# Performance work log

Measured on AMD Instinct MI355X. Metric: run time of the kernel, lower is better.

The kernel has to match this reference:

```python
import jax, jax.numpy as jnp
import numpy as np
from jax import lax

N = 1024          # n_ligand == n_receptor == feature dim (required by broadcast in source)
D = 1024          # gnn_input_dim == gnn_output_dim
H = 32            # hopi_output_dim
C = 32            # cnn_channels


def setup_inputs() -> dict:
    key = jax.random.key(0)
    ks = jax.random.split(key, 24)
    s = 0.02
    inp = {
        "ligand_node_features": jax.random.normal(ks[0], (N, D), jnp.float32),
        "ligand_edge_features": jax.random.normal(ks[1], (N, D), jnp.float32),
        "ligand_adjacency": jax.random.uniform(ks[2], (N, N), jnp.float32),
        "receptor_node_features": jax.random.normal(ks[3], (N, D), jnp.float32),
        "receptor_edge_features": jax.random.normal(ks[4], (N, D), jnp.float32),
        "receptor_adjacency": jax.random.uniform(ks[5], (N, N), jnp.float32),
        # GNNLayer params (shared between ligand and receptor, as in source)
        "Wn": jax.random.normal(ks[6], (D, D), jnp.float32) * s,
        "bn": jax.random.normal(ks[7], (D,), jnp.float32) * s,
        "We": jax.random.normal(ks[8], (D, D), jnp.float32) * s,
        "be": jax.random.normal(ks[9], (D,), jnp.float32) * s,
        "Wa": jax.random.normal(ks[10], (1, D), jnp.float32) * s,
        "ba": jax.random.normal(ks[11], (1,), jnp.float32) * s,
        # HighOrderPairwiseInteraction: Linear(2*D -> H)
        "W_hopi": jax.random.normal(ks[12], (H, 2 * D), jnp.float32) * s,
        "b_hopi": jax.random.normal(ks[13], (H,), jnp.float32) * s,
        # CNN tail
        "conv1_w": jax.random.normal(ks[14], (C, H, 3, 3), jnp.float32) * s,
        "conv1_b": jax.random.normal(ks[15], (C,), jnp.float32) * s,
        "conv2_w": jax.random.normal(ks[16], (C, C, 3, 3), jnp.float32) * s,
        "conv2_b": jax.random.normal(ks[17], (C,), jnp.float32) * s,
        "conv3_w": jax.random.normal(ks[18], (1, C, 1, 1), jnp.float32) * s,
        "conv3_b": jax.random.normal(ks[19], (1,), jnp.float32) * s,
    }
    return inp


def _gnn(nf, ef, Wn, bn, We, be, Wa, ba):
    # aggregated: [N, D]
    agg = jnp.tanh(nf @ Wn.T + bn + ef @ We.T + be)
    scores = agg @ Wa.T + ba                      # [N, 1]
    attn = jax.nn.softmax(scores, axis=1)         # softmax over size-1 dim -> ones (faithful)
    weighted = jnp.sum(agg * attn, axis=1)        # [N]
    return nf + weighted                          # [N,D] + [N] broadcasts over last dim (D == N)


def _conv(x, w, b):
    y = lax.conv_general_dilated(x, w, (1, 1), "SAME",
                                 dimension_numbers=("NCHW", "OIHW", "NCHW"))
    return y + b[None, :, None, None]


def reference(ligand_node_features, ligand_edge_features, ligand_adjacency,
              receptor_node_features, receptor_edge_features, receptor_adjacency,
              Wn, bn, We, be, Wa, ba, W_hopi, b_hopi,
              conv1_w, conv1_b, conv2_w, conv2_b, conv3_w, conv3_b):
    lig = _gnn(ligand_node_features, ligand_edge_features, Wn, bn, We, be, Wa, ba)
    rec = _gnn(receptor_node_features, receptor_edge_features, Wn, bn, We, be, Wa, ba)

    # HOPI: interactions[i, j] = Linear(cat(lig[i], rec[j])) == lig[i] @ Wl.T + rec[j] @ Wr.T + b
    Wl, Wr = W_hopi[:, :D], W_hopi[:, D:]
    lig_p = lig @ Wl.T                            # [N, H]
    rec_p = rec @ Wr.T                            # [N, H]
    interactions = lig_p[:, None, :] + rec_p[None, :, :] + b_hopi  # [N, N, H]

    x = jnp.transpose(interactions, (2, 0, 1))[None]  # [1, H, N, N]
    x = jax.nn.relu(_conv(x, conv1_w, conv1_b))
    x = jax.nn.relu(_conv(x, conv2_w, conv2_b))
    x = _conv(x, conv3_w, conv3_b)                # [1, 1, N, N]
    return x[0, 0]                                # [N, N]
```

## Files before the change

kernel.cpp:

```cpp
#include <hip/hip_runtime.h>


typedef _Float16 half8 __attribute__((ext_vector_type(8)));
typedef _Float16 half4 __attribute__((ext_vector_type(4)));
typedef float    f32x4 __attribute__((ext_vector_type(4)));

__device__ __forceinline__ short f2h_bits(float f){
    _Float16 h = (_Float16)f;
    return __builtin_bit_cast(short, h);
}
__device__ __forceinline__ half8 pack2(const float4& x, const float4& y){
    half8 r;
    r[0] = (_Float16)x.x; r[1] = (_Float16)x.y;
    r[2] = (_Float16)x.z; r[3] = (_Float16)x.w;
    r[4] = (_Float16)y.x; r[5] = (_Float16)y.y;
    r[6] = (_Float16)y.z; r[7] = (_Float16)y.w;
    return r;
}
__device__ __forceinline__ half4 pack4(const float4& x){
    half4 r;
    r[0] = (_Float16)x.x; r[1] = (_Float16)x.y;
    r[2] = (_Float16)x.z; r[3] = (_Float16)x.w;
    return r;
}
__device__ __forceinline__ float tanh_fast(float x){
    float e = __expf(2.f * x);
    return 1.f - 2.f / (e + 1.f);
}

#define SWZ(c) ((((c) >> 1) & 3) << 3)

#define GNN_LOAD(AV, BV, KBN) {                                              \
    const int kbn_ = (KBN) & 2047;                                           \
    const float* Asrc_ = (kbn_ < 1024) ? A0 : A1;                            \
    const float* Bsrc_ = (kbn_ < 1024) ? Wn : We;                            \
    const int kk_ = kbn_ & 1023;                                             \
    const float* ap_ = Asrc_ + (size_t)(j0 + arow) * 1024 + kk_ + akc;       \
    const float* bp_ = Bsrc_ + (size_t)(d0 + brow) * 1024 + kk_ + bkc;       \
    AV[0] = *reinterpret_cast<const float4*>(ap_);                           \
    AV[1] = *reinterpret_cast<const float4*>(ap_ + 4);                       \
    AV[2] = *reinterpret_cast<const float4*>(ap_ + 8);                       \
    AV[3] = *reinterpret_cast<const float4*>(ap_ + 12);                      \
    BV[0] = *reinterpret_cast<const float4*>(bp_);                           \
    BV[1] = *reinterpret_cast<const float4*>(bp_ + 4);                       \
}

#define GNN_STAGE(AV, BV) {                                                  \
    const int ga_ = (t & 3) * 2;                                             \
    const int sa_ = arow & 7;                                                \
    *reinterpret_cast<half8*>(&As[arow * 64 + ((ga_    ) ^ sa_) * 8]) = pack2(AV[0], AV[1]); \
    *reinterpret_cast<half8*>(&As[arow * 64 + ((ga_ + 1) ^ sa_) * 8]) = pack2(AV[2], AV[3]); \
    *reinterpret_cast<half8*>(&Bs[brow * 64 + ((t & 7) ^ (brow & 7)) * 8]) = pack2(BV[0], BV[1]); \
}

#define GNN_STAGE_W(KBS) {                                                   \
    const int r32_ = t >> 4;                                                 \
    const int kc_  = (t & 15) * 4;                                           \
    float4 wv_ = *reinterpret_cast<const float4*>(                           \
        Wp + (size_t)r32_ * 2048 + (KBS) + kc_);                             \
    *reinterpret_cast<half4*>(                                               \
        &Bs2[r32_ * 64 + ((((t & 15) >> 1)) ^ (r32_ & 7)) * 8 + (t & 1) * 4]) = pack4(wv_); \
}

#define GNN_MFMA() {                                                         \
    _Pragma("unroll")                                                        \
    for (int ks = 0; ks < 2; ++ks){                                          \
        half8 Af[2], Bf[2];                                                  \
        _Pragma("unroll")                                                    \
        for (int m = 0; m < 2; ++m){                                         \
            int row = wm * 32 + m * 16 + lr;                                 \
            int g   = ((ks * 4 + lg) ^ (row & 7)) * 8;                       \
            Af[m] = *reinterpret_cast<const half8*>(&As[row * 64 + g]);      \
        }                                                                    \
        _Pragma("unroll")                                                    \
        for (int n = 0; n < 2; ++n){                                         \
            int col = wn * 32 + n * 16 + lr;                                 \
            int g   = ((ks * 4 + lg) ^ (col & 7)) * 8;                       \
            Bf[n] = *reinterpret_cast<const half8*>(&Bs[col * 64 + g]);      \
        }                                                                    \
        _Pragma("unroll")                                                    \
        for (int m = 0; m < 2; ++m)                                          \
            _Pragma("unroll")                                                \
            for (int n = 0; n < 2; ++n)                                      \
                acc[m][n] = __builtin_amdgcn_mfma_f32_16x16x32_f16(          \
                    Af[m], Bf[n], acc[m][n], 0, 0, 0);                       \
    }                                                                        \
}

#define GNN_PMFMA() {                                                        \
    _Pragma("unroll")                                                        \
    for (int ks = 0; ks < 2; ++ks){                                          \
        int prow = wid * 16 + lr;                                            \
        half8 Af = *reinterpret_cast<const half8*>(                          \
            &As[prow * 64 + ((ks * 4 + lg) ^ (prow & 7)) * 8]);              \
        _Pragma("unroll")                                                    \
        for (int n = 0; n < 2; ++n){                                         \
            int col = n * 16 + lr;                                           \
            half8 Bf2 = *reinterpret_cast<const half8*>(                     \
                &Bs2[col * 64 + ((ks * 4 + lg) ^ (col & 7)) * 8]);           \
            pacc[n] = __builtin_amdgcn_mfma_f32_16x16x32_f16(                \
                Af, Bf2, pacc[n], 0, 0, 0);                                  \
        }                                                                    \
    }                                                                        \
}

__global__ __launch_bounds__(512) void gnn_kernel(
    const float* __restrict__ lig_nf, const float* __restrict__ lig_ef,
    const float* __restrict__ rec_nf, const float* __restrict__ rec_ef,
    const float* __restrict__ Wn, const float* __restrict__ We,
    const float* __restrict__ bn, const float* __restrict__ be,
    const float* __restrict__ W_hopi,
    float* __restrict__ part,
    short* __restrict__ Pw)
{
    __shared__ __attribute__((aligned(16))) short As[128 * 64];
    __shared__ __attribute__((aligned(16))) short Bs[64 * 64];
    __shared__ __attribute__((aligned(16))) short Bs2[32 * 64];
    __shared__ float red[128][2];

    const int t  = threadIdx.x;
    const int cx = blockIdx.z;
    const float* A0 = cx ? rec_nf : lig_nf;
    const float* A1 = cx ? rec_ef : lig_ef;
    const float* Wp = W_hopi + (cx ? 1024 : 0);
    const int j0 = blockIdx.x * 128;
    const int d0 = blockIdx.y * 64;
    const bool doP = (blockIdx.y == 0);

    const int wid  = t >> 6;
    const int wm   = wid >> 1;
    const int wn   = wid & 1;
    const int lane = t & 63;
    const int lr   = lane & 15;
    const int lg   = lane >> 4;

    f32x4 acc[2][2];
    #pragma unroll
    for (int m = 0; m < 2; ++m)
        #pragma unroll
        for (int n = 0; n < 2; ++n)
            acc[m][n] = (f32x4){0.f, 0.f, 0.f, 0.f};
    f32x4 pacc[2];
    pacc[0] = (f32x4){0.f, 0.f, 0.f, 0.f};
    pacc[1] = (f32x4){0.f, 0.f, 0.f, 0.f};

    const int arow = t >> 2;
    const int akc  = (t & 3) * 16;
    const int brow = t >> 3;
    const int bkc  = (t & 7) * 8;

    float4 avA[4], bvA[2], avB[4], bvB[2];
    GNN_LOAD(avA, bvA, 0);
    GNN_LOAD(avB, bvB, 64);

    for (int kb = 0; kb < 2048; kb += 128){
        const bool pA = doP && (kb < 1024);
        const bool pB = doP && (kb + 64 < 1024);
        __syncthreads();
        GNN_STAGE(avA, bvA);
        if (pA) GNN_STAGE_W(kb);
        GNN_LOAD(avA, bvA, kb + 128);
        __syncthreads();
        GNN_MFMA();
        if (pA) GNN_PMFMA();
        __syncthreads();
        GNN_STAGE(avB, bvB);
        if (pB) GNN_STAGE_W(kb + 64);
        GNN_LOAD(avB, bvB, kb + 192);
        __syncthreads();
        GNN_MFMA();
        if (pB) GNN_PMFMA();
    }

    float rowsum[2][4];
    #pragma unroll
    for (int m = 0; m < 2; ++m)
        #pragma unroll
        for (int jj = 0; jj < 4; ++jj) rowsum[m][jj] = 0.f;
    #pragma unroll
    for (int n = 0; n < 2; ++n){
        int d = d0 + wn * 32 + n * 16 + lr;
        float bias = bn[d] + be[d];
        #pragma unroll
        for (int m = 0; m < 2; ++m)
            #pragma unroll
            for (int jj = 0; jj < 4; ++jj)
                rowsum[m][jj] += tanh_fast(acc[m][n][jj] + bias);
    }
    #pragma unroll
    for (int mask = 1; mask < 16; mask <<= 1)
        #pragma unroll
        for (int m = 0; m < 2; ++m)
            #pragma unroll
            for (int jj = 0; jj < 4; ++jj)
                rowsum[m][jj] += __shfl_xor(rowsum[m][jj], mask);
    __syncthreads();
    if (lr == 0){
        #pragma unroll
        for (int m = 0; m < 2; ++m)
            #pragma unroll
            for (int jj = 0; jj < 4; ++jj)
                red[wm * 32 + m * 16 + lg * 4 + jj][wn] = rowsum[m][jj];
    }
    __syncthreads();
    if (t < 128)
        part[(size_t)cx * 16384 + (size_t)blockIdx.y * 1024 + j0 + t]
            = red[t][0] + red[t][1];

    if (doP){
        #pragma unroll
        for (int n = 0; n < 2; ++n)
            #pragma unroll
            for (int jj = 0; jj < 4; ++jj){
                int grow = j0 + wid * 16 + lg * 4 + jj;
                Pw[(size_t)cx * 32768 + (size_t)grow * 32 + n * 16 + lr]
                    = f2h_bits(pacc[n][jj]);
            }
    }
}

__global__ __launch_bounds__(512) void pp2_kernel(
    const float* __restrict__ W_hopi, const float* __restrict__ b_hopi,
    const float* __restrict__ w1, const float* __restrict__ b1,
    const float* __restrict__ w2,
    const float* __restrict__ part, const short* __restrict__ Pw,
    float* __restrict__ Kp, short* __restrict__ U16, short* __restrict__ V16,
    short* __restrict__ w2f16)
{
    __shared__ __attribute__((aligned(16))) char smem[47232];
    const int t = threadIdx.x;
    const int role = blockIdx.x;

    if (role < 32){
        short* Pz = reinterpret_cast<short*>(smem);
        short* Ws = reinterpret_cast<short*>(smem + 5376);

        const int cx = role >> 4;
        const int r0 = (role & 15) * 64;
        short* O = cx ? V16 : U16;
        const short* Psrc = Pw + (size_t)cx * 32768;

        const int wid = t >> 6;
        const int lane = t & 63;
        const int lr = lane & 15;
        const int lg = lane >> 4;

        for (int idx = t; idx < 2112; idx += 512){
            int l = idx >> 5;
            int h = idx & 31;
            int gr = r0 - 1 + l;
            short v = 0;
            if ((unsigned)gr < 1024u) v = Psrc[(size_t)gr * 32 + h];
            Pz[l * 40 + h] = v;
        }

        #pragma unroll
        for (int q = 0; q < 2; ++q){
            int pr = t * 2 + q;
            int co = pr >> 5;
            int ci = pr & 31;
            const float* wp = w1 + co * 288 + ci * 9;
            float tap[9];
            #pragma unroll
            for (int e = 0; e < 9; ++e) tap[e] = wp[e];
            #pragma unroll
            for (int d = 0; d < 3; ++d){
                float ta, tb, tc;
                if (cx == 0){ ta = tap[d * 3 + 0]; tb = tap[d * 3 + 1]; tc = tap[d * 3 + 2]; }
                else        { ta = tap[0 + d];     tb = tap[3 + d];     tc = tap[6 + d]; }
                Ws[(0 * 32 + co) * 104 + d * 32 + ci] = f2h_bits(ta + tb + tc);
                Ws[(1 * 32 + co) * 104 + d * 32 + ci] = f2h_bits(tb + tc);
                Ws[(2 * 32 + co) * 104 + d * 32 + ci] = f2h_bits(ta + tb);
            }
        }
        __syncthreads();

        if (wid < 4){
            f32x4 uacc[3][2];
            #pragma unroll
            for (int cs = 0; cs < 3; ++cs)
                #pragma unroll
                for (int n = 0; n < 2; ++n)
                    uacc[cs][n] = (f32x4){0.f, 0.f, 0.f, 0.f};
            #pragma unroll
            for (int d = 0; d < 3; ++d){
                int ar = wid * 16 + lr;
                half8 Ap = *reinterpret_cast<const half8*>(
                    &Pz[(ar + d) * 40 + lg * 8]);
                #pragma unroll
                for (int cs = 0; cs < 3; ++cs)
                    #pragma unroll
                    for (int n = 0; n < 2; ++n){
                        half8 Bp = *reinterpret_cast<const half8*>(
                            &Ws[(cs * 32 + n * 16 + lr) * 104 + d * 32 + lg * 8]);
                        uacc[cs][n] = __builtin_amdgcn_mfma_f32_16x16x32_f16(
                            Ap, Bp, uacc[cs][n], 0, 0, 0);
                    }
            }
            #pragma unroll
            for (int cs = 0; cs < 3; ++cs)
                #pragma unroll
                for (int n = 0; n < 2; ++n)
                    #pragma unroll
                    for (int jj = 0; jj < 4; ++jj){
                        int grow = r0 + wid * 16 + lg * 4 + jj;
                        O[((size_t)(cs << 10) + grow) * 32 + n * 16 + lr]
                            = f2h_bits(uacc[cs][n][jj]);
                    }
        }
        return;
    }

    if (role == 33){
        #pragma unroll
        for (int q = 0; q < 18; ++q){
            int e = t + q * 512;
            int co  = e / 288;
            int rem = e - co * 288;
            int ci  = rem / 9;
            int tap = rem - ci * 9;
            w2f16[(tap * 32 + co) * 32 + (ci ^ SWZ(co))] = f2h_bits(w2[e]);
        }
        return;
    }

    float* ws_l = reinterpret_cast<float*>(smem);
    float* ws_r = reinterpret_cast<float*>(smem + 4096);
    float* red  = reinterpret_cast<float*>(smem + 8192);
    float* cvs  = reinterpret_cast<float*>(smem + 10240);
    float* w1s  = reinterpret_cast<float*>(smem + 10368);

    #pragma unroll
    for (int q = 0; q < 5; ++q){
        int i4 = t + q * 512;
        if (i4 < 2304)
            *reinterpret_cast<float4*>(&w1s[i4 * 4]) =
                *reinterpret_cast<const float4*>(w1 + i4 * 4);
    }
    for (int j = t; j < 1024; j += 512){
        float sl = 0.f, sr = 0.f;
        #pragma unroll
        for (int b = 0; b < 16; ++b){
            sl += part[b * 1024 + j];
            sr += part[16384 + b * 1024 + j];
        }
        ws_l[j] = sl; ws_r[j] = sr;
    }
    __syncthreads();
    {
        const int h = t & 31;
        const int seg = t >> 5;
        const float* wl = W_hopi + (size_t)h * 2048 + seg * 64;
        const float* wr = wl + 1024;
        float s = 0.f;
        #pragma unroll 8
        for (int j = 0; j < 64; j += 4){
            float4 a = *reinterpret_cast<const float4*>(wl + j);
            float4 b = *reinterpret_cast<const float4*>(wr + j);
            const float* l = &ws_l[seg * 64 + j];
            const float* r = &ws_r[seg * 64 + j];
            s = fmaf(l[0], a.x, s); s = fmaf(l[1], a.y, s);
            s = fmaf(l[2], a.z, s); s = fmaf(l[3], a.w, s);
            s = fmaf(r[0], b.x, s); s = fmaf(r[1], b.y, s);
            s = fmaf(r[2], b.z, s); s = fmaf(r[3], b.w, s);
        }
        red[t] = s;
    }
    __syncthreads();
    if (t < 32){
        float tot = b_hopi[t];
        #pragma unroll
        for (int g = 0; g < 16; ++g) tot += red[g * 32 + t];
        cvs[t] = tot;
    }
    __syncthreads();
    for (int e = t; e < 288; e += 512){
        int co  = e & 31;
        int cse = e >> 5;
        int yc  = cse / 3, xc = cse - yc * 3;
        float sum = b1[co];
        for (int ci = 0; ci < 32; ++ci){
            const float* wp = &w1s[co * 288 + ci * 9];
            float t00 = wp[0], t01 = wp[1], t02 = wp[2];
            float t10 = wp[3], t11 = wp[4], t12 = wp[5];
            float t20 = wp[6], t21 = wp[7], t22 = wp[8];
            float r0, r1, r2;
            if (xc == 0){ r0 = t00+t01+t02; r1 = t10+t11+t12; r2 = t20+t21+t22; }
            else if (xc == 1){ r0 = t01+t02; r1 = t11+t12; r2 = t21+t22; }
            else { r0 = t00+t01; r1 = t10+t11; r2 = t20+t21; }
            float wsum = (yc == 0) ? (r0+r1+r2) : ((yc == 1) ? (r1+r2) : (r0+r1));
            sum = fmaf(cvs[ci], wsum, sum);
        }
        Kp[cse * 32 + co] = sum;
    }
}

__global__ __launch_bounds__(512) void conv_kernel(
    const short* __restrict__ U16, const short* __restrict__ V16,
    const float* __restrict__ Kp, const short* __restrict__ w2f16,
    const float* __restrict__ b2,
    const float* __restrict__ w3, const float* __restrict__ b3,
    float* __restrict__ outp)
{
    __shared__ __attribute__((aligned(16))) short ys[18 * 18 * 32];
    __shared__ __attribute__((aligned(16))) short wB[9 * 32 * 32];

    const int t    = threadIdx.x;
    const int oy0  = blockIdx.y * 16;
    const int ox0  = blockIdx.x * 16;
    const int wid  = t >> 6;
    const int lane = t & 63;
    const int lr   = lane & 15;
    const int lg   = lane >> 4;

    {
        const uint4* src = reinterpret_cast<const uint4*>(w2f16);
        uint4* dst = reinterpret_cast<uint4*>(wB);
        #pragma unroll
        for (int e = t; e < 1152; e += 512)
            dst[e] = src[e];
    }
    const bool interior = (blockIdx.x >= 1) & (blockIdx.x <= 62) &
                          (blockIdx.y >= 1) & (blockIdx.y <= 62);
    if (interior){
        const int cp = (t & 7) * 4;
        half4 k00;
        {
            float4 kf = *reinterpret_cast<const float4*>(&Kp[cp]);
            k00[0] = (_Float16)kf.x; k00[1] = (_Float16)kf.y;
            k00[2] = (_Float16)kf.z; k00[3] = (_Float16)kf.w;
        }
        #pragma unroll
        for (int pass = 0; pass < 6; ++pass){
            int idx = t + pass * 512;
            if (idx < 2592){
                int po  = idx >> 3;
                int ryo = po / 18;
                int rxo = po - ryo * 18;
                int gy = oy0 - 1 + ryo, gx = ox0 - 1 + rxo;
                half4 u = *reinterpret_cast<const half4*>(&U16[gy * 32 + cp]);
                half4 v = *reinterpret_cast<const half4*>(&V16[gx * 32 + cp]);
                half4 r = u + v + k00;
                #pragma unroll
                for (int e = 0; e < 4; ++e)
                    r[e] = r[e] > (_Float16)0.f ? r[e] : (_Float16)0.f;
                *reinterpret_cast<half4*>(&ys[po * 32 + (cp ^ SWZ(rxo))]) = r;
            }
        }
    } else {
        #pragma unroll
        for (int pass = 0; pass < 6; ++pass){
            int idx = t + pass * 512;
            if (idx < 2592){
                int po  = idx >> 3;
                int cp  = (idx & 7) * 4;
                int ryo = po / 18;
                int rxo = po - ryo * 18;
                int gy = oy0 - 1 + ryo, gx = ox0 - 1 + rxo;
                half4 h = {(_Float16)0.f, (_Float16)0.f, (_Float16)0.f, (_Float16)0.f};
                if ((unsigned)gy < 1024u && (unsigned)gx < 1024u){
                    int yc = (gy == 0) ? 1 : ((gy == 1023) ? 2 : 0);
                    int xc = (gx == 0) ? 1 : ((gx == 1023) ? 2 : 0);
                    half4 u = *reinterpret_cast<const half4*>(
                        &U16[((size_t)(xc << 10) + gy) * 32 + cp]);
                    half4 v = *reinterpret_cast<const half4*>(
                        &V16[((size_t)(yc << 10) + gx) * 32 + cp]);
                    float4 k = *reinterpret_cast<const float4*>(&Kp[(yc * 3 + xc) * 32 + cp]);
                    h[0] = (_Float16)fmaxf((float)u[0] + (float)v[0] + k.x, 0.f);
                    h[1] = (_Float16)fmaxf((float)u[1] + (float)v[1] + k.y, 0.f);
                    h[2] = (_Float16)fmaxf((float)u[2] + (float)v[2] + k.z, 0.f);
                    h[3] = (_Float16)fmaxf((float)u[3] + (float)v[3] + k.w, 0.f);
                }
                *reinterpret_cast<half4*>(&ys[po * 32 + (cp ^ SWZ(rxo))]) = h;
            }
        }
    }
    __syncthreads();

    {
        half8 Bf[2][9];
        float bias[2], w3v[2];
        #pragma unroll
        for (int n = 0; n < 2; ++n){
            int co = n * 16 + lr;
            bias[n] = b2[co];
            w3v[n]  = w3[co];
            #pragma unroll
            for (int tap = 0; tap < 9; ++tap)
                Bf[n][tap] = *reinterpret_cast<const half8*>(
                    &wB[(tap * 32 + co) * 32 + ((lg * 8) ^ SWZ(co))]);
        }
        const float b3v = b3[0];
        for (int s = wid; s < 16; s += 8){
            int p  = s * 16 + lr;
            int ry = p >> 4;
            int rx = p & 15;
            f32x4 acc0 = {0.f, 0.f, 0.f, 0.f};
            f32x4 acc1 = {0.f, 0.f, 0.f, 0.f};
            #pragma unroll
            for (int tap = 0; tap < 9; ++tap){
                const int dy = tap / 3, dx = tap - (tap / 3) * 3;
                int pix = (ry + dy) * 18 + rx + dx;
                half8 A = *reinterpret_cast<const half8*>(
                    &ys[pix * 32 + ((lg * 8) ^ SWZ(rx + dx))]);
                acc0 = __builtin_amdgcn_mfma_f32_16x16x32_f16(A, Bf[0][tap], acc0, 0, 0, 0);
                acc1 = __builtin_amdgcn_mfma_f32_16x16x32_f16(A, Bf[1][tap], acc1, 0, 0, 0);
            }
            float part[4];
            #pragma unroll
            for (int j = 0; j < 4; ++j)
                part[j] = w3v[0] * fmaxf(acc0[j] + bias[0], 0.f)
                        + w3v[1] * fmaxf(acc1[j] + bias[1], 0.f);
            #pragma unroll
            for (int m = 1; m < 16; m <<= 1)
                #pragma unroll
                for (int j = 0; j < 4; ++j)
                    part[j] += __shfl_xor(part[j], m);
            if (lr == 0){
                float4 o = make_float4(part[0] + b3v, part[1] + b3v,
                                       part[2] + b3v, part[3] + b3v);
                *reinterpret_cast<float4*>(outp + (size_t)(oy0 + s) * 1024 + ox0 + lg * 4) = o;
            }
        }
    }
}

extern "C" void kernel_launch(void* const* d_in, const int* in_sizes, int n_in,
                              void* d_out, int out_size, void* d_ws, size_t ws_size,
                              hipStream_t stream)
{
    const float* lig_nf = (const float*)d_in[0];
    const float* lig_ef = (const float*)d_in[1];
    const float* rec_nf = (const float*)d_in[3];
    const float* rec_ef = (const float*)d_in[4];
    const float* Wn     = (const float*)d_in[6];
    const float* bn     = (const float*)d_in[7];
    const float* We     = (const float*)d_in[8];
    const float* be     = (const float*)d_in[9];
    const float* W_hopi = (const float*)d_in[12];
    const float* b_hopi = (const float*)d_in[13];
    const float* w1     = (const float*)d_in[14];
    const float* b1     = (const float*)d_in[15];
    const float* w2     = (const float*)d_in[16];
    const float* b2     = (const float*)d_in[17];
    const float* w3     = (const float*)d_in[18];
    const float* b3     = (const float*)d_in[19];
    float* outp = (float*)d_out;

    float* part  = (float*)d_ws;
    short* Pw    = (short*)((char*)d_ws + 131072);
    float* Kp    = (float*)((char*)d_ws + 393216);
    short* U16   = (short*)((char*)d_ws + 394368);
    short* V16   = (short*)((char*)d_ws + 590976);
    short* w2f16 = (short*)((char*)d_ws + 787584);

    dim3 g1(8, 16, 2);
    gnn_kernel<<<g1, 512, 0, stream>>>(lig_nf, lig_ef, rec_nf, rec_ef,
                                       Wn, We, bn, be, W_hopi, part, Pw);
    pp2_kernel<<<34, 512, 0, stream>>>(W_hopi, b_hopi, w1, b1, w2,
                                       part, Pw, Kp, U16, V16, w2f16);
    dim3 g3(64, 64);
    conv_kernel<<<g3, 512, 0, stream>>>(U16, V16, Kp, w2f16, b2, w3, b3, outp);
}
```

Before: 118.3 us.

## Split GNN K-loop by projection phase and parallelize HOPI constant reduction

The GNN main loop is specialized into a doP branch with separate halves (with and without the projection MFMA) and a non-projection branch, removing per-iteration predicate checks. The single-block reduction that summed part rows and dotted them with W_hopi is spread across 16 blocks writing partial sums, and a new one-block kfin kernel finishes the constant and conv1 kernel-sum work. This aims to shorten the serial tail of pp2, at the cost of an extra kernel launch.

```diff
diff --git a/kernel.cpp b/kernel.cpp
--- a/kernel.cpp
+++ b/kernel.cpp
@@ -153,23 +153,48 @@
     GNN_LOAD(avA, bvA, 0);
     GNN_LOAD(avB, bvB, 64);
 
-    for (int kb = 0; kb < 2048; kb += 128){
-        const bool pA = doP && (kb < 1024);
-        const bool pB = doP && (kb + 64 < 1024);
-        __syncthreads();
-        GNN_STAGE(avA, bvA);
-        if (pA) GNN_STAGE_W(kb);
-        GNN_LOAD(avA, bvA, kb + 128);
-        __syncthreads();
-        GNN_MFMA();
-        if (pA) GNN_PMFMA();
-        __syncthreads();
-        GNN_STAGE(avB, bvB);
-        if (pB) GNN_STAGE_W(kb + 64);
-        GNN_LOAD(avB, bvB, kb + 192);
-        __syncthreads();
-        GNN_MFMA();
-        if (pB) GNN_PMFMA();
+    if (doP){
+        for (int kb = 0; kb < 1024; kb += 128){
+            __syncthreads();
+            GNN_STAGE(avA, bvA);
+            GNN_STAGE_W(kb);
+            GNN_LOAD(avA, bvA, kb + 128);
+            __syncthreads();
+            GNN_MFMA();
+            GNN_PMFMA();
+            __syncthreads();
+            GNN_STAGE(avB, bvB);
+            GNN_STAGE_W(kb + 64);
+            GNN_LOAD(avB, bvB, kb + 192);
+            __syncthreads();
+            GNN_MFMA();
+            GNN_PMFMA();
+        }
+        for (int kb = 1024; kb < 2048; kb += 128){
+            __syncthreads();
+            GNN_STAGE(avA, bvA);
+            GNN_LOAD(avA, bvA, kb + 128);
+            __syncthreads();
+            GNN_MFMA();
+            __syncthreads();
+            GNN_STAGE(avB, bvB);
+            GNN_LOAD(avB, bvB, kb + 192);
+            __syncthreads();
+            GNN_MFMA();
+        }
+    } else {
+        for (int kb = 0; kb < 2048; kb += 128){
+            __syncthreads();
+            GNN_STAGE(avA, bvA);
+            GNN_LOAD(avA, bvA, kb + 128);
+            __syncthreads();
+            GNN_MFMA();
+            __syncthreads();
+            GNN_STAGE(avB, bvB);
+            GNN_LOAD(avB, bvB, kb + 192);
+            __syncthreads();
+            GNN_MFMA();
+        }
     }
 
     float rowsum[2][4];
@@ -220,11 +245,11 @@
 }
 
 __global__ __launch_bounds__(512) void pp2_kernel(
-    const float* __restrict__ W_hopi, const float* __restrict__ b_hopi,
-    const float* __restrict__ w1, const float* __restrict__ b1,
-    const float* __restrict__ w2,
+    const float* __restrict__ W_hopi,
+    const float* __restrict__ w1, const float* __restrict__ w2,
     const float* __restrict__ part, const short* __restrict__ Pw,
-    float* __restrict__ Kp, short* __restrict__ U16, short* __restrict__ V16,
+    float* __restrict__ cpart,
+    short* __restrict__ U16, short* __restrict__ V16,
     short* __restrict__ w2f16)
 {
     __shared__ __attribute__((aligned(16))) char smem[47232];
@@ -311,7 +336,7 @@
         return;
     }
 
-    if (role == 33){
+    if (role == 48){
         #pragma unroll
         for (int q = 0; q < 18; ++q){
             int e = t + q * 512;
@@ -324,11 +349,55 @@
         return;
     }
 
-    float* ws_l = reinterpret_cast<float*>(smem);
-    float* ws_r = reinterpret_cast<float*>(smem + 4096);
-    float* red  = reinterpret_cast<float*>(smem + 8192);
-    float* cvs  = reinterpret_cast<float*>(smem + 10240);
-    float* w1s  = reinterpret_cast<float*>(smem + 10368);
+    {
+        float* ws_l = reinterpret_cast<float*>(smem);
+        float* ws_r = reinterpret_cast<float*>(smem + 256);
+        float* red  = reinterpret_cast<float*>(smem + 512);
+
+        const int q  = role - 32;
+        const int jb = q * 64;
+
+        if (t < 64){
+            int j = jb + t;
+            float sl = 0.f, sr = 0.f;
+            #pragma unroll
+            for (int b = 0; b < 16; ++b){
+                sl += part[b * 1024 + j];
+                sr += part[16384 + b * 1024 + j];
+            }
+            ws_l[t] = sl; ws_r[t] = sr;
+        }
+        __syncthreads();
+
+        const int h = t >> 4;
+        const int g = t & 15;
+        const float* wl = W_hopi + (size_t)h * 2048 + jb + g * 4;
+        const float* wr = wl + 1024;
+        float4 a = *reinterpret_cast<const float4*>(wl);
+        float4 b = *reinterpret_cast<const float4*>(wr);
+        const float* l = &ws_l[g * 4];
+        const float* r = &ws_r[g * 4];
+        float s = l[0] * a.x + l[1] * a.y + l[2] * a.z + l[3] * a.w
+                + r[0] * b.x + r[1] * b.y + r[2] * b.z + r[3] * b.w;
+        red[t] = s;
+        __syncthreads();
+        if (t < 32){
+            float tot = 0.f;
+            #pragma unroll
+            for (int gg = 0; gg < 16; ++gg) tot += red[t * 16 + gg];
+            cpart[q * 32 + t] = tot;
+        }
+    }
+}
+
+__global__ __launch_bounds__(512) void kfin_kernel(
+    const float* __restrict__ b_hopi, const float* __restrict__ w1,
+    const float* __restrict__ b1, const float* __restrict__ cpart,
+    float* __restrict__ Kp)
+{
+    __shared__ float cvs[32];
+    __shared__ float w1s[9216];
+    const int t = threadIdx.x;
 
     #pragma unroll
     for (int q = 0; q < 5; ++q){
@@ -337,40 +406,10 @@
             *reinterpret_cast<float4*>(&w1s[i4 * 4]) =
                 *reinterpret_cast<const float4*>(w1 + i4 * 4);
     }
-    for (int j = t; j < 1024; j += 512){
-        float sl = 0.f, sr = 0.f;
-        #pragma unroll
-        for (int b = 0; b < 16; ++b){
-            sl += part[b * 1024 + j];
-            sr += part[16384 + b * 1024 + j];
-        }
-        ws_l[j] = sl; ws_r[j] = sr;
-    }
-    __syncthreads();
-    {
-        const int h = t & 31;
-        const int seg = t >> 5;
-        const float* wl = W_hopi + (size_t)h * 2048 + seg * 64;
-        const float* wr = wl + 1024;
-        float s = 0.f;
-        #pragma unroll 8
-        for (int j = 0; j < 64; j += 4){
-            float4 a = *reinterpret_cast<const float4*>(wl + j);
-            float4 b = *reinterpret_cast<const float4*>(wr + j);
-            const float* l = &ws_l[seg * 64 + j];
-            const float* r = &ws_r[seg * 64 + j];
-            s = fmaf(l[0], a.x, s); s = fmaf(l[1], a.y, s);
-            s = fmaf(l[2], a.z, s); s = fmaf(l[3], a.w, s);
-            s = fmaf(r[0], b.x, s); s = fmaf(r[1], b.y, s);
-            s = fmaf(r[2], b.z, s); s = fmaf(r[3], b.w, s);
-        }
-        red[t] = s;
-    }
-    __syncthreads();
     if (t < 32){
         float tot = b_hopi[t];
         #pragma unroll
-        for (int g = 0; g < 16; ++g) tot += red[g * 32 + t];
+        for (int q = 0; q < 16; ++q) tot += cpart[q * 32 + t];
         cvs[t] = tot;
     }
     __syncthreads();
@@ -549,6 +588,7 @@
 
     float* part  = (float*)d_ws;
     short* Pw    = (short*)((char*)d_ws + 131072);
+    float* cpart = (float*)((char*)d_ws + 262144);
     float* Kp    = (float*)((char*)d_ws + 393216);
     short* U16   = (short*)((char*)d_ws + 394368);
     short* V16   = (short*)((char*)d_ws + 590976);
@@ -557,8 +597,9 @@
     dim3 g1(8, 16, 2);
     gnn_kernel<<<g1, 512, 0, stream>>>(lig_nf, lig_ef, rec_nf, rec_ef,
                                        Wn, We, bn, be, W_hopi, part, Pw);
-    pp2_kernel<<<34, 512, 0, stream>>>(W_hopi, b_hopi, w1, b1, w2,
-                                       part, Pw, Kp, U16, V16, w2f16);
+    pp2_kernel<<<49, 512, 0, stream>>>(W_hopi, w1, w2, part, Pw,
+                                       cpart, U16, V16, w2f16);
+    kfin_kernel<<<1, 512, 0, stream>>>(b_hopi, w1, b1, cpart, Kp);
     dim3 g3(64, 64);
     conv_kernel<<<g3, 512, 0, stream>>>(U16, V16, Kp, w2f16, b2, w3, b3, outp);
 }
```

Measured after the change: 111.5 us. 5.8% less time.
